# Optimization experiments

Hardware: AMD Instinct MI355X
Metric: run time of the kernel (lower is better)

Reference implementation:

```python
import jax, jax.numpy as jnp
import numpy as np

LAG = 24      # lag (months of 20 days) in the train window
STEP = 20     # days per rebalancing step
ANNUAL = 252.0


def setup_inputs() -> dict:
    key = jax.random.key(0)
    Y = jax.random.normal(key, (20480, 128), dtype=jnp.float32) * 0.01  # daily returns
    a = jnp.full((1,), 0.997, dtype=jnp.float32)                        # EWMA decay param
    logridge = jnp.full((1,), float(np.log(1e-5)), dtype=jnp.float32)   # log ridge param
    return {"Y": Y, "a": a, "logridge": logridge}


def reference(Y, a, logridge):
    n, p = Y.shape
    W = n // STEP - LAG            # number of rolling windows (1000)
    T = LAG * STEP                 # train window length (480)
    a0 = a[0]
    ridge = jnp.exp(logridge[0])

    # EWMA weights: w_t = a^(T-1-t) (most recent day has weight 1), normalized to sum T
    expo = jnp.arange(T - 1, -1, -1, dtype=Y.dtype)
    w = a0 ** expo
    w = w / w.sum() * T
    wsum = w.sum()
    denom = 1.0 - (w * w).sum() / (T * T)   # bias correction (w**2 / T**2).sum()
    ones_p = jnp.ones((p,), Y.dtype)

    def per_window(j):
        # train: Y[(i-lag)*20 : i*20] with i = j + LAG  ->  rows [j*20, j*20+T)
        Yt = jax.lax.dynamic_slice(Y, (j * STEP, 0), (T, p))
        # test: Y[i*20 : (i+1)*20]
        Yte = jax.lax.dynamic_slice(Y, ((j + LAG) * STEP, 0), (STEP, p))
        mean = (w[:, None] * Yt).sum(axis=0) / wsum          # [p]
        Yc = Yt - mean[None, :]                               # [T, p]
        Sigma = (Yc.T @ (w[:, None] * Yc)) / T / denom        # [p, p] weighted covariance
        lam, U = jnp.linalg.eigh(Sigma)
        Pmat = (U / (ridge + lam)[None, :]) @ U.T             # ridge-shrunk precision
        # GMV weights: P @ 1 / (1' P 1)
        v = Pmat @ ones_p
        wgt = v / (ones_p @ v)
        ret = Yte @ wgt                                       # [STEP] portfolio returns
        e = ret.sum()                                         # cumulative test return
        s = (ret * ret).mean()                                # realized daily variance
        return e, s

    e_all, s_all = jax.vmap(per_window)(jnp.arange(W))
    vol = jnp.sqrt(s_all.mean() * ANNUAL)
    mu = e_all.mean() / STEP * ANNUAL
    sharpe = mu / vol
    return vol, mu, sharpe
```

## Files before the change

kernel.cpp:

```cpp
#include <hip/hip_runtime.h>
#include <math.h>

#define P 128
#define T_WIN 480
#define STEPD 20
#define LAG_W 24
#define NITER 16
#define SEG 64
#define PACK 8448
#define PCHUNK 33

#define SBW_OFF 986
#define PW20_OFF 1024
#define AINVT_OFF 1280

__device__ __forceinline__ int tri_off(int r) {
  const int a = r >> 2, b = r & 3;
  return ((a + 1) * (2 * a + b)) << 2;
}

__global__ __launch_bounds__(512) void weights_kernel(const float* __restrict__ a,
                                                      float* __restrict__ wbuf) {
  __shared__ double redd[512];
  const int t = threadIdx.x;
  const double la = log((double)a[0]);
  const double u = (t < T_WIN) ? exp((double)(T_WIN - 1 - t) * la) : 0.0;
  redd[t] = u;
  __syncthreads();
  for (int off = 256; off > 0; off >>= 1) {
    if (t < off) redd[t] += redd[t + off];
    __syncthreads();
  }
  const double S = redd[0];
  __syncthreads();
  redd[t] = u * u;
  __syncthreads();
  for (int off = 256; off > 0; off >>= 1) {
    if (t < off) redd[t] += redd[t + off];
    __syncthreads();
  }
  const double Su2 = redd[0];
  if (t < T_WIN) {
    const double wn = u / S * (double)T_WIN;
    wbuf[t] = (float)wn;
    wbuf[T_WIN + t] = (float)sqrt(wn);
  }
  if (t == 0) {
    wbuf[960] = (float)(1.0 - Su2 / (S * S));
    wbuf[961] = (float)S;
  }
  if (t < LAG_W) wbuf[962 + t] = (float)exp((double)(STEPD * (LAG_W - 1 - t)) * la);
  if (t < STEPD) wbuf[SBW_OFF + t] = (float)exp(0.5 * (double)(STEPD - 1 - t) * la);
  if (t < 151) wbuf[PW20_OFF + t] = (float)exp((double)(20 * t) * la);
  if (t < SEG) wbuf[AINVT_OFF + t] = (float)exp(-(double)(20 * t) * la);
}

__global__ __launch_bounds__(256) void cblocks_kernel(const float* __restrict__ Y,
                                                      const float* __restrict__ wbuf,
                                                      float* __restrict__ cvec,
                                                      float* __restrict__ Call, int K) {
  const int k = blockIdx.x;
  const int tid = threadIdx.x;
  const int ti = tid >> 4, tj = tid & 15;
  __shared__ float st[STEPD][P];
  __shared__ float sbwsm[STEPD];
  if (tid < STEPD) sbwsm[tid] = wbuf[SBW_OFF + tid];
  __syncthreads();
  const float* __restrict__ Yb = Y + (size_t)k * STEPD * P;
  for (int i = tid; i < STEPD * P / 4; i += 256) {
    float4 v = ((const float4*)Yb)[i];
    const float sw = sbwsm[i >> 5];
    v.x *= sw; v.y *= sw; v.z *= sw; v.w *= sw;
    ((float4*)&st[0][0])[i] = v;
  }
  __syncthreads();

  float acc[8][8];
#pragma unroll
  for (int u = 0; u < 8; ++u)
#pragma unroll
    for (int v = 0; v < 8; ++v) acc[u][v] = 0.0f;

#pragma unroll 4
  for (int t = 0; t < STEPD; ++t) {
    float af[8], bf[8];
    *(float4*)(af)     = *(const float4*)&st[t][ti * 4];
    *(float4*)(af + 4) = *(const float4*)&st[t][64 + ti * 4];
    *(float4*)(bf)     = *(const float4*)&st[t][tj * 4];
    *(float4*)(bf + 4) = *(const float4*)&st[t][64 + tj * 4];
#pragma unroll
    for (int u = 0; u < 8; ++u)
#pragma unroll
      for (int v = 0; v < 8; ++v) acc[u][v] += af[u] * bf[v];
  }

  float* __restrict__ Ck = Call + (size_t)k * PACK;
#pragma unroll
  for (int u = 0; u < 8; ++u) {
    const int r = (u < 4) ? (ti * 4 + u) : (64 + ti * 4 + u - 4);
    const int offr = tri_off(r);
    if (tj * 4 <= r) {
      float4 o0;
      o0.x = acc[u][0]; o0.y = acc[u][1]; o0.z = acc[u][2]; o0.w = acc[u][3];
      *(float4*)(Ck + offr + tj * 4) = o0;
    }
    if (64 + tj * 4 <= r) {
      float4 o1;
      o1.x = acc[u][4]; o1.y = acc[u][5]; o1.z = acc[u][6]; o1.w = acc[u][7];
      *(float4*)(Ck + offr + 64 + tj * 4) = o1;
    }
  }
  if (tid < P) {
    float s = 0.0f;
    for (int t = 0; t < STEPD; ++t) s += sbwsm[t] * st[t][tid];
    cvec[(size_t)k * P + tid] = s;
  }
}

__global__ __launch_bounds__(256) void scan_kernel(float* __restrict__ Call,
                                                   const float* __restrict__ wbuf) {
  __shared__ float asm_[SEG];
  const int tid = threadIdx.x;
  const int seg = blockIdx.x / PCHUNK;
  const int chunk = blockIdx.x - seg * PCHUNK;
  if (tid < SEG) asm_[tid] = wbuf[AINVT_OFF + tid];
  __syncthreads();
  const int e = chunk * 256 + tid;
  float* __restrict__ base = Call + ((size_t)seg * SEG) * PACK + e;
  float g = 0.0f;
#pragma unroll 4
  for (int k = 0; k < SEG; ++k) {
    const float c = base[(size_t)k * PACK];
    g = fmaf(asm_[k], c, g);
    base[(size_t)k * PACK] = g;
  }
}

__global__ __launch_bounds__(128, 2) void window11_kernel(
    const float* __restrict__ Y, const float* __restrict__ wbuf,
    const float* __restrict__ logridge, const float* __restrict__ cvec,
    const float* __restrict__ Gall, float* __restrict__ e_all,
    float* __restrict__ s_all, int W) {
  const int bid = blockIdx.x;
  const int q = W >> 3, r8 = W & 7;
  const int xcd = bid & 7, idx = bid >> 3;
  const int j = ((xcd < r8) ? (xcd * (q + 1)) : (r8 * (q + 1) + (xcd - r8) * q)) + idx;

  const int tid = threadIdx.x;
  const int ti = tid >> 4, tj = tid & 15;
  const int lane = tid & 63;
  const int wv = tid >> 6;

  __shared__ float Gsm[PACK];
  __shared__ float rsm[P];
  __shared__ float wsm[P];
  __shared__ float vsm[P];
  __shared__ float meansm[P];
  __shared__ float coefsm[LAG_W];
  __shared__ float2 gd_wave[2];
  __shared__ float rs_wave[2];
  __shared__ float retd[STEPD];

  if (tid < LAG_W) coefsm[tid] = wbuf[962 + tid];
  __syncthreads();

  const float S = wbuf[961];
  const float denom = wbuf[960];
  const float ridge = expf(logridge[0]);

  int offR[16];
#pragma unroll
  for (int u = 0; u < 16; ++u) offR[u] = tri_off(ti * 16 + u);
  int colv[8], offC[8];
#pragma unroll
  for (int v = 0; v < 8; ++v) {
    colv[v] = (v < 4) ? (tj * 4 + v) : (64 + tj * 4 + (v - 4));
    offC[v] = tri_off(colv[v]);
  }

  int mats[3];
  float scls[3];
  int nm = 0;
  {
    const int o1 = j & ~(SEG - 1);
    const int end = j + 23;
    const int b = o1 + SEG;
    const float pA = wbuf[PW20_OFF + (end - o1)];
    if (end < b) {
      mats[nm] = end; scls[nm] = pA; ++nm;
      if (j > o1) { mats[nm] = j - 1; scls[nm] = -pA; ++nm; }
    } else {
      const float pB2 = wbuf[PW20_OFF + (end - b)];
      mats[nm] = b - 1; scls[nm] = pA; ++nm;
      if (j > o1) { mats[nm] = j - 1; scls[nm] = -pA; ++nm; }
      mats[nm] = end; scls[nm] = pB2; ++nm;
    }
  }

  {
    float4* __restrict__ Gsm4 = (float4*)Gsm;
    if (nm == 3) {
      const float cf0 = scls[0], cf1 = scls[1], cf2 = scls[2];
      const float4* __restrict__ G0 = (const float4*)(Gall + (size_t)mats[0] * PACK);
      const float4* __restrict__ G1 = (const float4*)(Gall + (size_t)mats[1] * PACK);
      const float4* __restrict__ G2 = (const float4*)(Gall + (size_t)mats[2] * PACK);
      for (int i = tid; i < PACK / 4; i += 128) {
        const float4 a0 = G0[i];
        const float4 a1 = G1[i];
        const float4 a2 = G2[i];
        float4 o;
        o.x = cf0 * a0.x + cf1 * a1.x + cf2 * a2.x;
        o.y = cf0 * a0.y + cf1 * a1.y + cf2 * a2.y;
        o.z = cf0 * a0.z + cf1 * a1.z + cf2 * a2.z;
        o.w = cf0 * a0.w + cf1 * a1.w + cf2 * a2.w;
        Gsm4[i] = o;
      }
    } else {
      const float cf0 = scls[0];
      const float cf1 = (nm > 1) ? scls[1] : 0.0f;
      const float4* __restrict__ G0 = (const float4*)(Gall + (size_t)mats[0] * PACK);
      const float4* __restrict__ G1 = (const float4*)(Gall + (size_t)mats[(nm > 1) ? 1 : 0] * PACK);
      for (int i = tid; i < PACK / 4; i += 128) {
        const float4 a0 = G0[i];
        const float4 a1 = G1[i];
        float4 o;
        o.x = cf0 * a0.x + cf1 * a1.x;
        o.y = cf0 * a0.y + cf1 * a1.y;
        o.z = cf0 * a0.z + cf1 * a1.z;
        o.w = cf0 * a0.w + cf1 * a1.w;
        Gsm4[i] = o;
      }
    }
  }

  {
    float s = 0.0f;
    for (int m = 0; m < LAG_W; ++m) s += coefsm[m] * cvec[(size_t)(j + m) * P + tid];
    meansm[tid] = s;
    rsm[tid] = 1.0f;
  }
  __syncthreads();

  float acc[16][8];
  {
    const float sc1 = 1.0f / (S * denom);
    const float sc2 = 1.0f / (S * S * denom);
#pragma unroll
    for (int u = 0; u < 16; ++u) {
      const int r = ti * 16 + u;
      const int offr = offR[u];
      const float mr = meansm[r] * sc2;
#pragma unroll
      for (int v = 0; v < 8; ++v) {
        const int c = colv[v];
        const int idxe = (c <= r) ? (offr + c) : (offC[v] + r);
        float mval = Gsm[idxe] * sc1 - mr * meansm[c];
        if (r == c) mval += ridge;
        acc[u][v] = mval;
      }
    }
  }
  __syncthreads();

  float xo = 0.0f, ro = 1.0f, po = 0.0f, so = 0.0f;
  float gam_old = 1.0f, alp_old = 1.0f;

  for (int it = 0; it < NITER; ++it) {
    const float4 p0 = *(const float4*)&rsm[tj * 4];
    const float4 p1 = *(const float4*)&rsm[64 + tj * 4];
    float pv[8] = {p0.x, p0.y, p0.z, p0.w, p1.x, p1.y, p1.z, p1.w};
    float ap[16];
#pragma unroll
    for (int u = 0; u < 16; ++u) {
      float s = 0.0f;
#pragma unroll
      for (int v = 0; v < 8; ++v) s += acc[u][v] * pv[v];
      ap[u] = s;
    }
#pragma unroll
    for (int m = 1; m <= 8; m <<= 1) {
#pragma unroll
      for (int u = 0; u < 16; ++u) ap[u] += __shfl_xor(ap[u], m);
    }
    if (tj == 0) {
      float gp = 0.0f, dp = 0.0f;
#pragma unroll
      for (int u = 0; u < 16; ++u) {
        const int r = ti * 16 + u;
        const float rv = rsm[r];
        wsm[r] = ap[u];
        gp = fmaf(rv, rv, gp);
        dp = fmaf(ap[u], rv, dp);
      }
      gp += __shfl_down(gp, 16); dp += __shfl_down(dp, 16);
      gp += __shfl_down(gp, 32); dp += __shfl_down(dp, 32);
      if (lane == 0) { gd_wave[wv].x = gp; gd_wave[wv].y = dp; }
    }
    __syncthreads();

    const float gam = gd_wave[0].x + gd_wave[1].x;
    const float del = gd_wave[0].y + gd_wave[1].y;
    float bet, alp;
    if (it == 0) { bet = 0.0f; alp = gam / del; }
    else {
      bet = gam / gam_old;
      alp = gam / (del - bet * gam / alp_old);
    }
    gam_old = gam; alp_old = alp;

    const float wv_c = wsm[tid];
    po = ro + bet * po;
    so = wv_c + bet * so;
    xo += alp * po;
    ro -= alp * so;
    rsm[tid] = ro;
    __syncthreads();
  }

  vsm[tid] = xo;
  float sv = xo;
#pragma unroll
  for (int m = 32; m > 0; m >>= 1) sv += __shfl_down(sv, m);
  if (lane == 0) rs_wave[wv] = sv;
  __syncthreads();
  const float sumv = rs_wave[0] + rs_wave[1];

  const float* __restrict__ Yte = Y + (size_t)(j + LAG_W) * STEPD * P;
  for (int d = wv; d < STEPD; d += 2) {
    float pp = Yte[(size_t)d * P + lane] * vsm[lane] +
               Yte[(size_t)d * P + 64 + lane] * vsm[64 + lane];
    for (int off = 32; off > 0; off >>= 1) pp += __shfl_down(pp, off);
    if (lane == 0) retd[d] = pp;
  }
  __syncthreads();

  if (tid == 0) {
    const float invs = 1.0f / sumv;
    float e = 0.0f, s = 0.0f;
#pragma unroll
    for (int d = 0; d < STEPD; ++d) {
      const float rr = retd[d] * invs;
      e += rr; s += rr * rr;
    }
    e_all[j] = e;
    s_all[j] = s * (1.0f / (float)STEPD);
  }
}

__global__ __launch_bounds__(256, 2) void window_fallback(
    const float* __restrict__ Y, const float* __restrict__ wbuf,
    const float* __restrict__ logridge, float* __restrict__ e_all,
    float* __restrict__ s_all, int W) {
  const int j = blockIdx.x;
  const int tid = threadIdx.x;
  const int ti = tid >> 4;
  const int tj = tid & 15;

  __shared__ float Msm[P][P + 1];
  __shared__ float wsm[T_WIN];
  __shared__ float swsm[T_WIN];
  __shared__ float meansm[P];
  __shared__ float red[256];
  __shared__ float retd[STEPD];
  __shared__ float zsm[P];
  __shared__ float vsm[P];
  __shared__ float bsm[P];

  float* stage = &Msm[0][0];

  for (int t = tid; t < T_WIN; t += 256) {
    wsm[t] = wbuf[t];
    swsm[t] = wbuf[T_WIN + t];
  }
  if (tid < P) bsm[tid] = 1.0f;
  const float denom = wbuf[960];
  const float ridge = expf(logridge[0]);
  __syncthreads();

  const float* __restrict__ Ywin = Y + (size_t)j * STEPD * P;
  {
    const int col = tid & 127;
    const int half = tid >> 7;
    float m = 0.0f;
    const int t0 = half * (T_WIN / 2), t1 = t0 + T_WIN / 2;
    for (int t = t0; t < t1; ++t) m += wsm[t] * Ywin[(size_t)t * P + col];
    red[tid] = m;
    __syncthreads();
    if (tid < P) meansm[tid] = (red[tid] + red[tid + 128]) * (1.0f / (float)T_WIN);
    __syncthreads();
  }

  float acc[8][8];
#pragma unroll
  for (int u = 0; u < 8; ++u)
#pragma unroll
    for (int v = 0; v < 8; ++v) acc[u][v] = 0.0f;

  for (int c = 0; c < T_WIN / 32; ++c) {
    __syncthreads();
#pragma unroll
    for (int i = 0; i < 4; ++i) {
      const int idx = i * 1024 + tid * 4;
      float4 v = *(const float4*)(Ywin + (size_t)c * 32 * P + idx);
      const float sw = swsm[c * 32 + (idx >> 7)];
      v.x *= sw; v.y *= sw; v.z *= sw; v.w *= sw;
      *(float4*)(stage + idx) = v;
    }
    __syncthreads();
#pragma unroll 4
    for (int t = 0; t < 32; ++t) {
      const float* rowp = stage + t * P;
      float af[8], bf[8];
      *(float4*)(af) = *(const float4*)(rowp + ti * 8);
      *(float4*)(af + 4) = *(const float4*)(rowp + ti * 8 + 4);
      *(float4*)(bf) = *(const float4*)(rowp + tj * 8);
      *(float4*)(bf + 4) = *(const float4*)(rowp + tj * 8 + 4);
#pragma unroll
      for (int u = 0; u < 8; ++u)
#pragma unroll
        for (int v = 0; v < 8; ++v) acc[u][v] += af[u] * bf[v];
    }
  }
  __syncthreads();

  const float invTd = 1.0f / ((float)T_WIN * denom);
#pragma unroll
  for (int u = 0; u < 8; ++u) {
    const int r = ti * 8 + u;
    const float mr = meansm[r];
#pragma unroll
    for (int v = 0; v < 8; ++v) {
      const int cc = tj * 8 + v;
      float m = (acc[u][v] - (float)T_WIN * mr * meansm[cc]) * invTd;
      if (r == cc) m += ridge;
      Msm[r][cc] = m;
    }
  }
  __syncthreads();

  for (int k = 0; k < P; ++k) {
    const float dkk = Msm[k][k];
    const float sq = sqrtf(dkk);
    const float invd = 1.0f / sq;
    if (tid == 0) Msm[k][k] = sq;
    const int i = k + 1 + tid;
    if (i < P) Msm[i][k] *= invd;
    __syncthreads();
    const int nrem = P - 1 - k;
    for (int ii = ti; ii < nrem; ii += 16) {
      const int ri = k + 1 + ii;
      const float Lik = Msm[ri][k];
      for (int jj = tj; jj < nrem; jj += 16) {
        const int cj = k + 1 + jj;
        Msm[ri][cj] -= Lik * Msm[cj][k];
      }
    }
    __syncthreads();
  }

  for (int k = 0; k < P; ++k) {
    const float zk = bsm[k] / Msm[k][k];
    if (tid == 0) zsm[k] = zk;
    const int i = k + 1 + tid;
    if (i < P) bsm[i] -= Msm[i][k] * zk;
    __syncthreads();
  }
  for (int k = P - 1; k >= 0; --k) {
    const float vk = zsm[k] / Msm[k][k];
    if (tid == 0) vsm[k] = vk;
    if (tid < k) zsm[tid] -= Msm[k][tid] * vk;
    __syncthreads();
  }

  red[tid] = (tid < P) ? vsm[tid] : 0.0f;
  __syncthreads();
  for (int off = 128; off > 0; off >>= 1) {
    if (tid < off) red[tid] += red[tid + off];
    __syncthreads();
  }

  const float* __restrict__ Yte = Y + (size_t)(j + LAG_W) * STEPD * P;
  const int wv = tid >> 6;
  const int lane = tid & 63;
  for (int d = wv; d < STEPD; d += 4) {
    float pp = Yte[(size_t)d * P + lane] * vsm[lane] +
               Yte[(size_t)d * P + 64 + lane] * vsm[64 + lane];
    for (int off = 32; off > 0; off >>= 1) pp += __shfl_down(pp, off);
    if (lane == 0) retd[d] = pp;
  }
  __syncthreads();

  if (tid == 0) {
    const float invs = 1.0f / red[0];
    float e = 0.0f, s = 0.0f;
#pragma unroll
    for (int d = 0; d < STEPD; ++d) {
      const float r = retd[d] * invs;
      e += r;
      s += r * r;
    }
    e_all[j] = e;
    s_all[j] = s * (1.0f / (float)STEPD);
  }
}

__global__ __launch_bounds__(256) void final_kernel(const float* __restrict__ e_all,
                                                    const float* __restrict__ s_all,
                                                    float* __restrict__ out, int W) {
  __shared__ float r1[256], r2[256];
  const int tid = threadIdx.x;
  float e = 0.0f, s = 0.0f;
  for (int i = tid; i < W; i += 256) {
    e += e_all[i];
    s += s_all[i];
  }
  r1[tid] = e;
  r2[tid] = s;
  __syncthreads();
  for (int off = 128; off > 0; off >>= 1) {
    if (tid < off) {
      r1[tid] += r1[tid + off];
      r2[tid] += r2[tid + off];
    }
    __syncthreads();
  }
  if (tid == 0) {
    const float vol = sqrtf(r2[0] / (float)W * 252.0f);
    const float mu = r1[0] / (float)W / (float)STEPD * 252.0f;
    out[0] = vol;
    out[1] = mu;
    out[2] = mu / vol;
  }
}

extern "C" void kernel_launch(void* const* d_in, const int* in_sizes, int n_in,
                              void* d_out, int out_size, void* d_ws, size_t ws_size,
                              hipStream_t stream) {
  const float* Y = (const float*)d_in[0];
  const float* a = (const float*)d_in[1];
  const float* logridge = (const float*)d_in[2];
  float* out = (float*)d_out;

  const int n = in_sizes[0] / P;
  const int K = n / STEPD;
  const int W = K - LAG_W;

  float* ws = (float*)d_ws;
  float* wbuf = ws;
  float* e_all = ws + 2048;
  float* s_all = ws + 3072;
  float* cvec = ws + 4096;
  float* Gall = ws + 4096 + (size_t)K * P;

  const size_t need = ((size_t)4096 + (size_t)K * P + (size_t)K * PACK) * sizeof(float);

  weights_kernel<<<1, 512, 0, stream>>>(a, wbuf);
  if (ws_size >= need && (n % STEPD) == 0 && W > 0 && W <= 1024 && (K % SEG) == 0) {
    cblocks_kernel<<<K, 256, 0, stream>>>(Y, wbuf, cvec, Gall, K);
    scan_kernel<<<(K / SEG) * PCHUNK, 256, 0, stream>>>(Gall, wbuf);
    window11_kernel<<<W, 128, 0, stream>>>(Y, wbuf, logridge, cvec, Gall, e_all, s_all, W);
  } else {
    window_fallback<<<W, 256, 0, stream>>>(Y, wbuf, logridge, e_all, s_all, W);
  }
  final_kernel<<<1, 256, 0, stream>>>(e_all, s_all, out, W);
}
```

Baseline: 92.17 us.

## Drop weights kernel, compute EWMA constants inline, cut CG iterations to 14

Removes the separate single-block weights kernel. Each consumer kernel now computes its EWMA powers and the normalization constants itself, using a closed-form geometric series in double precision, which saves one launch and the dependency on it. The CG solver iteration count drops from 16 to 14, and the residual reads in the dot-product step become vectorized float4 loads with the wsm store split out. Fewer iterations can lower solver accuracy, and per-thread double exp/log adds some cost to every block.

```diff
diff --git a/kernel.cpp b/kernel.cpp
--- a/kernel.cpp
+++ b/kernel.cpp
@@ -5,58 +5,28 @@
 #define T_WIN 480
 #define STEPD 20
 #define LAG_W 24
-#define NITER 16
+#define NITER 14
 #define SEG 64
 #define PACK 8448
 #define PCHUNK 33
 
-#define SBW_OFF 986
-#define PW20_OFF 1024
-#define AINVT_OFF 1280
-
 __device__ __forceinline__ int tri_off(int r) {
   const int a = r >> 2, b = r & 3;
   return ((a + 1) * (2 * a + b)) << 2;
 }
 
-__global__ __launch_bounds__(512) void weights_kernel(const float* __restrict__ a,
-                                                      float* __restrict__ wbuf) {
-  __shared__ double redd[512];
-  const int t = threadIdx.x;
-  const double la = log((double)a[0]);
-  const double u = (t < T_WIN) ? exp((double)(T_WIN - 1 - t) * la) : 0.0;
-  redd[t] = u;
-  __syncthreads();
-  for (int off = 256; off > 0; off >>= 1) {
-    if (t < off) redd[t] += redd[t + off];
-    __syncthreads();
-  }
-  const double S = redd[0];
-  __syncthreads();
-  redd[t] = u * u;
-  __syncthreads();
-  for (int off = 256; off > 0; off >>= 1) {
-    if (t < off) redd[t] += redd[t + off];
-    __syncthreads();
-  }
-  const double Su2 = redd[0];
-  if (t < T_WIN) {
-    const double wn = u / S * (double)T_WIN;
-    wbuf[t] = (float)wn;
-    wbuf[T_WIN + t] = (float)sqrt(wn);
-  }
-  if (t == 0) {
-    wbuf[960] = (float)(1.0 - Su2 / (S * S));
-    wbuf[961] = (float)S;
-  }
-  if (t < LAG_W) wbuf[962 + t] = (float)exp((double)(STEPD * (LAG_W - 1 - t)) * la);
-  if (t < STEPD) wbuf[SBW_OFF + t] = (float)exp(0.5 * (double)(STEPD - 1 - t) * la);
-  if (t < 151) wbuf[PW20_OFF + t] = (float)exp((double)(20 * t) * la);
-  if (t < SEG) wbuf[AINVT_OFF + t] = (float)exp(-(double)(20 * t) * la);
+__device__ __forceinline__ void ewma_consts(float af, double& la, float& Sf, float& denomf) {
+  const double a = (double)af;
+  la = log(a);
+  const double A480 = exp(480.0 * la);
+  const double S = (1.0 - A480) / (1.0 - a);
+  const double Su2 = (1.0 - A480 * A480) / (1.0 - a * a);
+  Sf = (float)S;
+  denomf = (float)(1.0 - Su2 / (S * S));
 }
 
 __global__ __launch_bounds__(256) void cblocks_kernel(const float* __restrict__ Y,
-                                                      const float* __restrict__ wbuf,
+                                                      const float* __restrict__ aarg,
                                                       float* __restrict__ cvec,
                                                       float* __restrict__ Call, int K) {
   const int k = blockIdx.x;
@@ -64,7 +34,10 @@
   const int ti = tid >> 4, tj = tid & 15;
   __shared__ float st[STEPD][P];
   __shared__ float sbwsm[STEPD];
-  if (tid < STEPD) sbwsm[tid] = wbuf[SBW_OFF + tid];
+  if (tid < STEPD) {
+    const double la = log((double)aarg[0]);
+    sbwsm[tid] = (float)exp(0.5 * (double)(STEPD - 1 - tid) * la);
+  }
   __syncthreads();
   const float* __restrict__ Yb = Y + (size_t)k * STEPD * P;
   for (int i = tid; i < STEPD * P / 4; i += 256) {
@@ -118,12 +91,15 @@
 }
 
 __global__ __launch_bounds__(256) void scan_kernel(float* __restrict__ Call,
-                                                   const float* __restrict__ wbuf) {
+                                                   const float* __restrict__ aarg) {
   __shared__ float asm_[SEG];
   const int tid = threadIdx.x;
   const int seg = blockIdx.x / PCHUNK;
   const int chunk = blockIdx.x - seg * PCHUNK;
-  if (tid < SEG) asm_[tid] = wbuf[AINVT_OFF + tid];
+  if (tid < SEG) {
+    const double la = log((double)aarg[0]);
+    asm_[tid] = (float)exp(-(double)(20 * tid) * la);
+  }
   __syncthreads();
   const int e = chunk * 256 + tid;
   float* __restrict__ base = Call + ((size_t)seg * SEG) * PACK + e;
@@ -136,8 +112,8 @@
   }
 }
 
-__global__ __launch_bounds__(128, 2) void window11_kernel(
-    const float* __restrict__ Y, const float* __restrict__ wbuf,
+__global__ __launch_bounds__(128, 2) void window12_kernel(
+    const float* __restrict__ Y, const float* __restrict__ aarg,
     const float* __restrict__ logridge, const float* __restrict__ cvec,
     const float* __restrict__ Gall, float* __restrict__ e_all,
     float* __restrict__ s_all, int W) {
@@ -150,6 +126,7 @@
   const int ti = tid >> 4, tj = tid & 15;
   const int lane = tid & 63;
   const int wv = tid >> 6;
+  const int rowbase = ti * 16;
 
   __shared__ float Gsm[PACK];
   __shared__ float rsm[P];
@@ -161,16 +138,18 @@
   __shared__ float rs_wave[2];
   __shared__ float retd[STEPD];
 
-  if (tid < LAG_W) coefsm[tid] = wbuf[962 + tid];
-  __syncthreads();
-
-  const float S = wbuf[961];
-  const float denom = wbuf[960];
+  double la_d;
+  float S, denom;
+  ewma_consts(aarg[0], la_d, S, denom);
   const float ridge = expf(logridge[0]);
 
+  if (tid < LAG_W)
+    coefsm[tid] = (float)exp((double)(STEPD * (LAG_W - 1 - tid)) * la_d);
+  __syncthreads();
+
   int offR[16];
 #pragma unroll
-  for (int u = 0; u < 16; ++u) offR[u] = tri_off(ti * 16 + u);
+  for (int u = 0; u < 16; ++u) offR[u] = tri_off(rowbase + u);
   int colv[8], offC[8];
 #pragma unroll
   for (int v = 0; v < 8; ++v) {
@@ -185,12 +164,12 @@
     const int o1 = j & ~(SEG - 1);
     const int end = j + 23;
     const int b = o1 + SEG;
-    const float pA = wbuf[PW20_OFF + (end - o1)];
+    const float pA = (float)exp((double)(STEPD * (end - o1)) * la_d);
     if (end < b) {
       mats[nm] = end; scls[nm] = pA; ++nm;
       if (j > o1) { mats[nm] = j - 1; scls[nm] = -pA; ++nm; }
     } else {
-      const float pB2 = wbuf[PW20_OFF + (end - b)];
+      const float pB2 = (float)exp((double)(STEPD * (end - b)) * la_d);
       mats[nm] = b - 1; scls[nm] = pA; ++nm;
       if (j > o1) { mats[nm] = j - 1; scls[nm] = -pA; ++nm; }
       mats[nm] = end; scls[nm] = pB2; ++nm;
@@ -247,7 +226,7 @@
     const float sc2 = 1.0f / (S * S * denom);
 #pragma unroll
     for (int u = 0; u < 16; ++u) {
-      const int r = ti * 16 + u;
+      const int r = rowbase + u;
       const int offr = offR[u];
       const float mr = meansm[r] * sc2;
 #pragma unroll
@@ -283,14 +262,21 @@
       for (int u = 0; u < 16; ++u) ap[u] += __shfl_xor(ap[u], m);
     }
     if (tj == 0) {
+#pragma unroll
+      for (int u = 0; u < 16; ++u) wsm[rowbase + u] = ap[u];
+    }
+    {
+      const float4 r0 = *(const float4*)&rsm[rowbase];
+      const float4 r1 = *(const float4*)&rsm[rowbase + 4];
+      const float4 r2 = *(const float4*)&rsm[rowbase + 8];
+      const float4 r3 = *(const float4*)&rsm[rowbase + 12];
+      const float rv[16] = {r0.x, r0.y, r0.z, r0.w, r1.x, r1.y, r1.z, r1.w,
+                            r2.x, r2.y, r2.z, r2.w, r3.x, r3.y, r3.z, r3.w};
       float gp = 0.0f, dp = 0.0f;
 #pragma unroll
       for (int u = 0; u < 16; ++u) {
-        const int r = ti * 16 + u;
-        const float rv = rsm[r];
-        wsm[r] = ap[u];
-        gp = fmaf(rv, rv, gp);
-        dp = fmaf(ap[u], rv, dp);
+        gp = fmaf(rv[u], rv[u], gp);
+        dp = fmaf(ap[u], rv[u], dp);
       }
       gp += __shfl_down(gp, 16); dp += __shfl_down(dp, 16);
       gp += __shfl_down(gp, 32); dp += __shfl_down(dp, 32);
@@ -348,7 +334,7 @@
 }
 
 __global__ __launch_bounds__(256, 2) void window_fallback(
-    const float* __restrict__ Y, const float* __restrict__ wbuf,
+    const float* __restrict__ Y, const float* __restrict__ aarg,
     const float* __restrict__ logridge, float* __restrict__ e_all,
     float* __restrict__ s_all, int W) {
   const int j = blockIdx.x;
@@ -368,12 +354,15 @@
 
   float* stage = &Msm[0][0];
 
+  double la;
+  float S, denom;
+  ewma_consts(aarg[0], la, S, denom);
   for (int t = tid; t < T_WIN; t += 256) {
-    wsm[t] = wbuf[t];
-    swsm[t] = wbuf[T_WIN + t];
+    const double wn = exp((double)(T_WIN - 1 - t) * la) / (double)S * (double)T_WIN;
+    wsm[t] = (float)wn;
+    swsm[t] = (float)sqrt(wn);
   }
   if (tid < P) bsm[tid] = 1.0f;
-  const float denom = wbuf[960];
   const float ridge = expf(logridge[0]);
   __syncthreads();
 
@@ -546,21 +535,19 @@
   const int W = K - LAG_W;
 
   float* ws = (float*)d_ws;
-  float* wbuf = ws;
-  float* e_all = ws + 2048;
-  float* s_all = ws + 3072;
-  float* cvec = ws + 4096;
-  float* Gall = ws + 4096 + (size_t)K * P;
-
-  const size_t need = ((size_t)4096 + (size_t)K * P + (size_t)K * PACK) * sizeof(float);
-
-  weights_kernel<<<1, 512, 0, stream>>>(a, wbuf);
+  float* e_all = ws;
+  float* s_all = ws + 1024;
+  float* cvec = ws + 2048;
+  float* Gall = ws + 2048 + (size_t)K * P;
+
+  const size_t need = ((size_t)2048 + (size_t)K * P + (size_t)K * PACK) * sizeof(float);
+
   if (ws_size >= need && (n % STEPD) == 0 && W > 0 && W <= 1024 && (K % SEG) == 0) {
-    cblocks_kernel<<<K, 256, 0, stream>>>(Y, wbuf, cvec, Gall, K);
-    scan_kernel<<<(K / SEG) * PCHUNK, 256, 0, stream>>>(Gall, wbuf);
-    window11_kernel<<<W, 128, 0, stream>>>(Y, wbuf, logridge, cvec, Gall, e_all, s_all, W);
+    cblocks_kernel<<<K, 256, 0, stream>>>(Y, a, cvec, Gall, K);
+    scan_kernel<<<(K / SEG) * PCHUNK, 256, 0, stream>>>(Gall, a);
+    window12_kernel<<<W, 128, 0, stream>>>(Y, a, logridge, cvec, Gall, e_all, s_all, W);
   } else {
-    window_fallback<<<W, 256, 0, stream>>>(Y, wbuf, logridge, e_all, s_all, W);
+    window_fallback<<<W, 256, 0, stream>>>(Y, a, logridge, e_all, s_all, W);
   }
   final_kernel<<<1, 256, 0, stream>>>(e_all, s_all, out, W);
 }
```

Result: faster. 84.33 us (-8.5%).
